# Kernel tuning notes

Hardware: AMD Instinct MI355X
Metric: run time of the kernel (lower is better)

The kernel has to match this reference:

```python
import jax, jax.numpy as jnp
import numpy as np

HEADS = 8

def setup_inputs() -> dict:
    key = jax.random.key(0)
    ks = jax.random.split(key, 5)
    B, C, H, W = 2, 256, 64, 64
    dim = C
    x = jax.random.normal(ks[0], (B, C, H, W), dtype=jnp.float32)
    # Linear weights stored as [in, out] so y = x @ W + b
    w_qkv = jax.random.normal(ks[1], (dim, 3 * dim), dtype=jnp.float32) * (dim ** -0.5)
    b_qkv = jax.random.normal(ks[2], (3 * dim,), dtype=jnp.float32) * 0.02
    w_out = jax.random.normal(ks[3], (dim, dim), dtype=jnp.float32) * (dim ** -0.5)
    b_out = jax.random.normal(ks[4], (dim,), dtype=jnp.float32) * 0.02
    return {"x": x, "w_qkv": w_qkv, "b_qkv": b_qkv, "w_out": w_out, "b_out": b_out}

def reference(x, w_qkv, b_qkv, w_out, b_out):
    B, C, H, W = x.shape
    h = HEADS
    d = C // h
    scale = d ** -0.5
    # [B, C, H, W] -> [B, N, C]
    tokens = x.reshape(B, C, H * W).transpose(0, 2, 1)
    qkv = tokens @ w_qkv + b_qkv  # [B, N, 3C]
    q, k, v = jnp.split(qkv, 3, axis=-1)
    def to_heads(t):
        Bn, N, _ = t.shape
        return t.reshape(Bn, N, h, d).transpose(0, 2, 1, 3)  # [B, h, N, d]
    q, k, v = map(to_heads, (q, k, v))
    dots = jnp.einsum('bhnd,bhmd->bhnm', q, k) * scale  # [B, h, N, N]
    attn = jax.nn.softmax(dots, axis=-1)
    out = jnp.einsum('bhnm,bhmd->bhnd', attn, v)  # [B, h, N, d]
    out = out.transpose(0, 2, 1, 3).reshape(B, H * W, C)  # [B, N, C]
    out = out @ w_out + b_out
    return out.transpose(0, 2, 1).reshape(B, C, H, W)
```

## Files before the change

### kernel.cpp

```cpp
#include <hip/hip_runtime.h>

typedef __attribute__((ext_vector_type(8))) short s16x8;
typedef __attribute__((ext_vector_type(4))) short s16x4;
typedef __attribute__((ext_vector_type(4))) float f32x4;
typedef __attribute__((ext_vector_type(2))) unsigned u32x2;

#define MFMA32(a, b, c) __builtin_amdgcn_mfma_f32_16x16x32_bf16((a), (b), (c), 0, 0, 0)

#if __has_builtin(__builtin_amdgcn_mfma_f32_16x16x16bf16_1k)
#define MFMA16K(a, b, c) __builtin_amdgcn_mfma_f32_16x16x16bf16_1k((a), (b), (c), 0, 0, 0)
#else
#define MFMA16K(a, b, c) (c)
#endif

#if __has_builtin(__builtin_amdgcn_exp2f)
#define EXP2F(x) __builtin_amdgcn_exp2f(x)
#else
#define EXP2F(x) __exp2f(x)
#endif

#if __has_builtin(__builtin_amdgcn_rcpf)
#define RCPF(x) __builtin_amdgcn_rcpf(x)
#else
#define RCPF(x) (1.0f / (x))
#endif

#define SL2E 0.25507313f

__device__ __forceinline__ unsigned pkrne(float a, float b) {
  unsigned ua = __builtin_bit_cast(unsigned, a);
  unsigned ub = __builtin_bit_cast(unsigned, b);
  ua += 0x7FFFu + ((ua >> 16) & 1u);
  ub += 0x7FFFu + ((ub >> 16) & 1u);
  return __builtin_amdgcn_perm(ub, ua, 0x07060302u);
}

__device__ __forceinline__ unsigned pktrunc(float a, float b) {
  return __builtin_amdgcn_perm(__builtin_bit_cast(unsigned, b),
                               __builtin_bit_cast(unsigned, a), 0x07060302u);
}

__device__ __forceinline__ unsigned short bfr(float f) {
  unsigned u = __builtin_bit_cast(unsigned, f);
  u += 0x7FFFu + ((u >> 16) & 1u);
  return (unsigned short)(u >> 16);
}

__device__ __forceinline__ float bflo(unsigned u) {
  return __builtin_bit_cast(float, u << 16);
}
__device__ __forceinline__ float bfhi(unsigned u) {
  return __builtin_bit_cast(float, u & 0xFFFF0000u);
}

__global__ __launch_bounds__(256) void prep_kernel(
    const float* __restrict__ x, const float* __restrict__ wqkv,
    const float* __restrict__ wout, ushort* __restrict__ xbf,
    ushort* __restrict__ wT, ushort* __restrict__ woT) {
  const int t = threadIdx.x;
  const int sub = t & 15, grp = t >> 4;
  const int id = blockIdx.x;
  const float* src;
  ushort* dst;
  int src_ld, k0, n0;
  float sc = 1.f;
  if (id < 512) {
    int mt = id & 63, kt = (id >> 6) & 3, b = id >> 8;
    src = x + (size_t)b * 256 * 4096;
    src_ld = 4096;
    dst = xbf + (size_t)b * 4096 * 256;
    k0 = kt * 64;
    n0 = mt * 64;
  } else if (id < 560) {
    int r = id - 512, nt = r % 12, kt = r / 12;
    src = wqkv;
    src_ld = 768;
    dst = wT;
    k0 = kt * 64;
    n0 = nt * 64;
    if (n0 < 256) sc = SL2E;
  } else {
    int r = id - 560, nt = r & 3, kt = r >> 2;
    src = wout;
    src_ld = 256;
    dst = woT;
    k0 = kt * 64;
    n0 = nt * 64;
  }
  const int k = k0 + grp * 4;
  const int n = n0 + sub * 4;
  unsigned d0[4], d1[4];
#pragma unroll
  for (int i = 0; i < 4; ++i) {
    float4 v = *(const float4*)(src + (size_t)(k + i) * src_ld + n);
    d0[i] = pkrne(v.x * sc, v.y * sc);
    d1[i] = pkrne(v.z * sc, v.w * sc);
  }
  u32x2 r0 = {__builtin_amdgcn_perm(d0[1], d0[0], 0x05040100u),
              __builtin_amdgcn_perm(d0[3], d0[2], 0x05040100u)};
  u32x2 r1 = {__builtin_amdgcn_perm(d0[1], d0[0], 0x07060302u),
              __builtin_amdgcn_perm(d0[3], d0[2], 0x07060302u)};
  u32x2 r2 = {__builtin_amdgcn_perm(d1[1], d1[0], 0x05040100u),
              __builtin_amdgcn_perm(d1[3], d1[2], 0x05040100u)};
  u32x2 r3 = {__builtin_amdgcn_perm(d1[1], d1[0], 0x07060302u),
              __builtin_amdgcn_perm(d1[3], d1[2], 0x07060302u)};
  *(u32x2*)(dst + (size_t)(n + 0) * 256 + k) = r0;
  *(u32x2*)(dst + (size_t)(n + 1) * 256 + k) = r1;
  *(u32x2*)(dst + (size_t)(n + 2) * 256 + k) = r2;
  *(u32x2*)(dst + (size_t)(n + 3) * 256 + k) = r3;
}

__global__ __launch_bounds__(256) void qkv_kernel(
    const ushort* __restrict__ xbf, const ushort* __restrict__ wT,
    const float* __restrict__ bq, ushort* __restrict__ QG,
    ushort* __restrict__ KG, ushort* __restrict__ VtG) {
  __shared__ __align__(16) ushort Wl[64][40];
  __shared__ __align__(16) ushort Xl[128][40];
  const int t0 = blockIdx.x * 128;
  const int n0 = blockIdx.y * 64;
  const int t = threadIdx.x;
  const int wid = t >> 6, lane = t & 63;
  const int wy = wid >> 1, wx = wid & 1;
  const int quad = lane >> 4, l16 = lane & 15;
  f32x4 acc[2][4] = {};
  const int wr = t >> 2, wsg = t & 3;
  for (int k0 = 0; k0 < 256; k0 += 32) {
    __syncthreads();
    *(uint4*)&Wl[wr][wsg * 8] =
        *(const uint4*)(wT + (size_t)(n0 + wr) * 256 + k0 + wsg * 8);
#pragma unroll
    for (int i = 0; i < 2; ++i) {
      int fid = t + 256 * i, row = fid >> 2, seg = fid & 3;
      *(uint4*)&Xl[row][seg * 8] =
          *(const uint4*)(xbf + (size_t)(t0 + row) * 256 + k0 + seg * 8);
    }
    __syncthreads();
    s16x8 wf[2], xf[4];
#pragma unroll
    for (int i = 0; i < 2; ++i)
      wf[i] = *(const s16x8*)&Wl[32 * wy + 16 * i + l16][quad * 8];
#pragma unroll
    for (int j = 0; j < 4; ++j)
      xf[j] = *(const s16x8*)&Xl[64 * wx + 16 * j + l16][quad * 8];
#pragma unroll
    for (int i = 0; i < 2; ++i)
#pragma unroll
      for (int j = 0; j < 4; ++j) acc[i][j] = MFMA32(wf[i], xf[j], acc[i][j]);
  }
  if (n0 < 512) {
    ushort* dst = (n0 < 256) ? QG : KG;
    const float bsc = (n0 < 256) ? SL2E : 1.f;
#pragma unroll
    for (int i = 0; i < 2; ++i) {
      int nb = n0 + 32 * wy + 16 * i + 4 * quad;
      float4 b4 = *(const float4*)(bq + nb);
      float bx0 = b4.x * bsc, bx1 = b4.y * bsc, bx2 = b4.z * bsc,
            bx3 = b4.w * bsc;
      int h = ((nb & 255) >> 5);
      int dd0 = nb & 31;
#pragma unroll
      for (int j = 0; j < 4; ++j) {
        int tok = t0 + 64 * wx + 16 * j + l16;
        int b = tok >> 12, tokn = tok & 4095;
        u32x2 pk = {pkrne(acc[i][j][0] + bx0, acc[i][j][1] + bx1),
                    pkrne(acc[i][j][2] + bx2, acc[i][j][3] + bx3)};
        *(u32x2*)(dst + ((size_t)(b * 8 + h) * 4096 + tokn) * 32 + dd0) = pk;
      }
    }
  } else {
#pragma unroll
    for (int i = 0; i < 2; ++i) {
      int nb = n0 + 32 * wy + 16 * i + 4 * quad;
      float4 b4 = *(const float4*)(bq + nb);
      float bb[4] = {b4.x, b4.y, b4.z, b4.w};
#pragma unroll
      for (int r = 0; r < 4; ++r) {
        int nn = nb + r - 512;
        int h = nn >> 5, ddv = nn & 31;
        ushort* vrow = VtG + (size_t)(h * 32 + ddv) * 4096;
#pragma unroll
        for (int j = 0; j < 4; ++j) {
          int tok = t0 + 64 * wx + 16 * j + l16;
          int b = tok >> 12, tokn = tok & 4095;
          vrow[(size_t)b * 8 * 32 * 4096 + tokn] = bfr(acc[i][j][r] + bb[r]);
        }
      }
    }
  }
}

__global__ __launch_bounds__(256, 4) void attn_split(
    const ushort* __restrict__ QG, const ushort* __restrict__ KG,
    const ushort* __restrict__ VtG, ushort* __restrict__ OF0,
    ushort* __restrict__ OFb, float* __restrict__ LF) {
  __shared__ __align__(16) ushort Kl[2][64][40];
  __shared__ __align__(16) ushort Vl[2][32][72];
  const int id = blockIdx.x;
  const int bh = (id & 7) * 2 + ((id >> 3) & 1);
  const int q0 = ((id >> 4) & 15) * 256;
  const int sp = id >> 8;
  const int kt0 = sp * 16;
  const int t = threadIdx.x;
  const int wid = t >> 6, lane = t & 63;
  const int quad = lane >> 4, l16 = lane & 15;
  const size_t base = (size_t)bh * 4096 * 32;
  const ushort* qp = QG + base;
  const ushort* kp = KG + base;
  const ushort* vp = VtG + base;
  const int qw = q0 + 64 * wid;
  s16x8 qf[4];
#pragma unroll
  for (int f = 0; f < 4; ++f)
    qf[f] = *(const s16x8*)(qp + (size_t)(qw + 16 * f + l16) * 32 + quad * 8);
  const int kr = t >> 2, ks = t & 3;
  const int vr = t >> 3, vsg = t & 7;
  *(uint4*)&Kl[0][kr][ks * 8] =
      *(const uint4*)(kp + (size_t)(kt0 * 64 + kr) * 32 + ks * 8);
  *(uint4*)&Vl[0][vr][vsg * 8] =
      *(const uint4*)(vp + (size_t)vr * 4096 + kt0 * 64 + vsg * 8);
  const ushort* kpre = kp + (size_t)((kt0 + 1) * 64 + kr) * 32 + ks * 8;
  const ushort* vpre = vp + (size_t)vr * 4096 + (kt0 + 1) * 64 + vsg * 8;
  __syncthreads();
  f32x4 oA[4], oB[4], ol[4];
#pragma unroll
  for (int f = 0; f < 4; ++f) {
    oA[f] = f32x4{};
    oB[f] = f32x4{};
    ol[f] = f32x4{};
  }
  const f32x4 zero = {};
  const s16x4 ones = {(short)0x3F80, (short)0x3F80, (short)0x3F80,
                      (short)0x3F80};
  for (int i = 0; i < 16; ++i) {
    const int cur = i & 1;
    const bool more = (i + 1) < 16;
    uint4 kv, vv;
    if (more) {
      kv = *(const uint4*)kpre;
      vv = *(const uint4*)vpre;
      kpre += 2048;
      vpre += 64;
    }
#pragma unroll
    for (int nb = 0; nb < 4; ++nb) {
      s16x8 kf = *(const s16x8*)&Kl[cur][16 * nb + l16][quad * 8];
      s16x4 va = *(const s16x4*)&Vl[cur][l16][16 * nb + quad * 4];
      s16x4 vb = *(const s16x4*)&Vl[cur][16 + l16][16 * nb + quad * 4];
#pragma unroll
      for (int f = 0; f < 4; ++f) {
        f32x4 s = MFMA32(kf, qf[f], zero);
        u32x2 pu = {pktrunc(EXP2F(s[0]), EXP2F(s[1])),
                    pktrunc(EXP2F(s[2]), EXP2F(s[3]))};
        s16x4 pv = __builtin_bit_cast(s16x4, pu);
        oA[f] = MFMA16K(va, pv, oA[f]);
        oB[f] = MFMA16K(vb, pv, oB[f]);
        ol[f] = MFMA16K(ones, pv, ol[f]);
      }
    }
    if (more) {
      *(uint4*)&Kl[cur ^ 1][kr][ks * 8] = kv;
      *(uint4*)&Vl[cur ^ 1][vr][vsg * 8] = vv;
    }
    __syncthreads();
  }
  ushort* OFs = (sp == 0) ? OF0 : OFb + (size_t)(sp - 1) * 2097152;
  float* LFs = LF + (size_t)sp * 65536;
#pragma unroll
  for (int f = 0; f < 4; ++f) {
    const int tok = qw + 16 * f + l16;
    const size_t ob = ((size_t)bh * 4096 + tok) * 32;
    u32x2 wA = {pkrne(oA[f][0], oA[f][1]), pkrne(oA[f][2], oA[f][3])};
    u32x2 wB = {pkrne(oB[f][0], oB[f][1]), pkrne(oB[f][2], oB[f][3])};
    *(u32x2*)(OFs + ob + 4 * quad) = wA;
    *(u32x2*)(OFs + ob + 16 + 4 * quad) = wB;
    if (quad == 0) LFs[(size_t)bh * 4096 + tok] = ol[f][0];
  }
}

__global__ __launch_bounds__(256) void proj_split(
    const ushort* __restrict__ OF0, const ushort* __restrict__ OFb,
    const float* __restrict__ LF, const ushort* __restrict__ woT,
    const float* __restrict__ bo, float* __restrict__ out) {
  __shared__ __align__(16) ushort Wl[64][40];
  __shared__ __align__(16) ushort Xl[128][40];
  const int t0 = blockIdx.x * 128;
  const int c0 = blockIdx.y * 64;
  const int t = threadIdx.x;
  const int wid = t >> 6, lane = t & 63;
  const int wy = wid >> 1, wx = wid & 1;
  const int quad = lane >> 4, l16 = lane & 15;
  f32x4 acc[2][4] = {};
  const int wr = t >> 2, wsg = t & 3;
  const int c8 = (t & 7) * 4;
  for (int k0 = 0; k0 < 256; k0 += 32) {
    __syncthreads();
    *(uint4*)&Wl[wr][wsg * 8] =
        *(const uint4*)(woT + (size_t)(c0 + wr) * 256 + k0 + wsg * 8);
    const int hh = k0 >> 5;
#pragma unroll
    for (int p = 0; p < 4; ++p) {
      int row = 32 * p + (t >> 3);
      int tok = t0 + row, bb = tok >> 12, tokn = tok & 4095;
      size_t ro = (size_t)(bb * 8 + hh) * 4096 + tokn;
      size_t oi = ro * 32 + c8;
      uint2 a0 = *(const uint2*)(OF0 + oi);
      uint2 a1 = *(const uint2*)(OFb + oi);
      uint2 a2 = *(const uint2*)(OFb + 2097152 + oi);
      uint2 a3 = *(const uint2*)(OFb + 4194304 + oi);
      float l = (LF[ro] + LF[65536 + ro]) + (LF[131072 + ro] + LF[196608 + ro]);
      float inv = RCPF(l);
      f32x4 s;
      s[0] = (bflo(a0.x) + bflo(a1.x)) + (bflo(a2.x) + bflo(a3.x));
      s[1] = (bfhi(a0.x) + bfhi(a1.x)) + (bfhi(a2.x) + bfhi(a3.x));
      s[2] = (bflo(a0.y) + bflo(a1.y)) + (bflo(a2.y) + bflo(a3.y));
      s[3] = (bfhi(a0.y) + bfhi(a1.y)) + (bfhi(a2.y) + bfhi(a3.y));
      s *= inv;
      u32x2 pk = {pkrne(s[0], s[1]), pkrne(s[2], s[3])};
      *(u32x2*)&Xl[row][c8] = pk;
    }
    __syncthreads();
    s16x8 wf[2], xf[4];
#pragma unroll
    for (int i = 0; i < 2; ++i)
      wf[i] = *(const s16x8*)&Wl[32 * wy + 16 * i + l16][quad * 8];
#pragma unroll
    for (int j = 0; j < 4; ++j)
      xf[j] = *(const s16x8*)&Xl[64 * wx + 16 * j + l16][quad * 8];
#pragma unroll
    for (int i = 0; i < 2; ++i)
#pragma unroll
      for (int j = 0; j < 4; ++j) acc[i][j] = MFMA32(wf[i], xf[j], acc[i][j]);
  }
#pragma unroll
  for (int i = 0; i < 2; ++i) {
    int cb = c0 + 32 * wy + 16 * i + 4 * quad;
    float4 b4 = *(const float4*)(bo + cb);
    float bb[4] = {b4.x, b4.y, b4.z, b4.w};
#pragma unroll
    for (int j = 0; j < 4; ++j) {
      int tok = t0 + 64 * wx + 16 * j + l16;
      int b = tok >> 12, tokn = tok & 4095;
#pragma unroll
      for (int r = 0; r < 4; ++r)
        out[((size_t)(b * 256 + cb + r)) * 4096 + tokn] = acc[i][j][r] + bb[r];
    }
  }
}

extern "C" void kernel_launch(void* const* d_in, const int* in_sizes, int n_in,
                              void* d_out, int out_size, void* d_ws, size_t ws_size,
                              hipStream_t stream) {
  (void)in_sizes; (void)n_in; (void)out_size; (void)ws_size;
  const float* x = (const float*)d_in[0];
  const float* wq = (const float*)d_in[1];
  const float* bq = (const float*)d_in[2];
  const float* wo = (const float*)d_in[3];
  const float* bo = (const float*)d_in[4];
  float* out = (float*)d_out;
  ushort* ws = (ushort*)d_ws;
  ushort* xbf = ws;
  ushort* OF0 = ws;
  ushort* QG  = ws + 2097152;
  ushort* KG  = ws + 4194304;
  ushort* VtG = ws + 6291456;
  ushort* wT  = ws + 8388608;
  ushort* woT = ws + 8585216;
  ushort* OFb = ws + 8650752;
  float* LF = (float*)(ws + 14942208);
  prep_kernel<<<576, 256, 0, stream>>>(x, wq, wo, xbf, wT, woT);
  qkv_kernel<<<dim3(64, 12), 256, 0, stream>>>(xbf, wT, bq, QG, KG, VtG);
  attn_split<<<1024, 256, 0, stream>>>(QG, KG, VtG, OF0, OFb, LF);
  proj_split<<<dim3(64, 4), 256, 0, stream>>>(OF0, OFb, LF, woT, bo, out);
}
```

Before: 142.9 us.

## Load K/V fragments directly from global memory, dropping LDS staging and barriers

The attention kernel no longer stages K and V tiles through double-buffered shared memory with per-iteration __syncthreads. Each wave now reads its MFMA K and V fragments straight from global memory, relying on L1/L2 caching, with a per-block rotation of the key-tile order to spread accesses across blocks. The goal is to remove the LDS round trip and barrier stalls and to free LDS for occupancy. In exchange, each wave re-fetches the same K/V data its siblings fetch, and the strided V reads (4096-element row stride) may hit the cache poorly and raise global latency.

```diff
diff --git a/kernel.cpp b/kernel.cpp
--- a/kernel.cpp
+++ b/kernel.cpp
@@ -193,13 +193,12 @@
     const ushort* __restrict__ QG, const ushort* __restrict__ KG,
     const ushort* __restrict__ VtG, ushort* __restrict__ OF0,
     ushort* __restrict__ OFb, float* __restrict__ LF) {
-  __shared__ __align__(16) ushort Kl[2][64][40];
-  __shared__ __align__(16) ushort Vl[2][32][72];
   const int id = blockIdx.x;
   const int bh = (id & 7) * 2 + ((id >> 3) & 1);
   const int q0 = ((id >> 4) & 15) * 256;
   const int sp = id >> 8;
   const int kt0 = sp * 16;
+  const int rot = id & 15;
   const int t = threadIdx.x;
   const int wid = t >> 6, lane = t & 63;
   const int quad = lane >> 4, l16 = lane & 15;
@@ -212,15 +211,6 @@
 #pragma unroll
   for (int f = 0; f < 4; ++f)
     qf[f] = *(const s16x8*)(qp + (size_t)(qw + 16 * f + l16) * 32 + quad * 8);
-  const int kr = t >> 2, ks = t & 3;
-  const int vr = t >> 3, vsg = t & 7;
-  *(uint4*)&Kl[0][kr][ks * 8] =
-      *(const uint4*)(kp + (size_t)(kt0 * 64 + kr) * 32 + ks * 8);
-  *(uint4*)&Vl[0][vr][vsg * 8] =
-      *(const uint4*)(vp + (size_t)vr * 4096 + kt0 * 64 + vsg * 8);
-  const ushort* kpre = kp + (size_t)((kt0 + 1) * 64 + kr) * 32 + ks * 8;
-  const ushort* vpre = vp + (size_t)vr * 4096 + (kt0 + 1) * 64 + vsg * 8;
-  __syncthreads();
   f32x4 oA[4], oB[4], ol[4];
 #pragma unroll
   for (int f = 0; f < 4; ++f) {
@@ -231,21 +221,19 @@
   const f32x4 zero = {};
   const s16x4 ones = {(short)0x3F80, (short)0x3F80, (short)0x3F80,
                       (short)0x3F80};
+#pragma unroll 2
   for (int i = 0; i < 16; ++i) {
-    const int cur = i & 1;
-    const bool more = (i + 1) < 16;
-    uint4 kv, vv;
-    if (more) {
-      kv = *(const uint4*)kpre;
-      vv = *(const uint4*)vpre;
-      kpre += 2048;
-      vpre += 64;
-    }
+    const int kt = kt0 + ((i + rot) & 15);
+    const ushort* kbase = kp + (size_t)kt * 64 * 32;
+    const ushort* vbase = vp + kt * 64;
 #pragma unroll
     for (int nb = 0; nb < 4; ++nb) {
-      s16x8 kf = *(const s16x8*)&Kl[cur][16 * nb + l16][quad * 8];
-      s16x4 va = *(const s16x4*)&Vl[cur][l16][16 * nb + quad * 4];
-      s16x4 vb = *(const s16x4*)&Vl[cur][16 + l16][16 * nb + quad * 4];
+      s16x8 kf =
+          *(const s16x8*)(kbase + (size_t)(nb * 16 + l16) * 32 + quad * 8);
+      s16x4 va =
+          *(const s16x4*)(vbase + (size_t)l16 * 4096 + nb * 16 + quad * 4);
+      s16x4 vb = *(const s16x4*)(vbase + (size_t)(16 + l16) * 4096 + nb * 16 +
+                                 quad * 4);
 #pragma unroll
       for (int f = 0; f < 4; ++f) {
         f32x4 s = MFMA32(kf, qf[f], zero);
@@ -257,11 +245,6 @@
         ol[f] = MFMA16K(ones, pv, ol[f]);
       }
     }
-    if (more) {
-      *(uint4*)&Kl[cur ^ 1][kr][ks * 8] = kv;
-      *(uint4*)&Vl[cur ^ 1][vr][vsg * 8] = vv;
-    }
-    __syncthreads();
   }
   ushort* OFs = (sp == 0) ? OF0 : OFb + (size_t)(sp - 1) * 2097152;
   float* LFs = LF + (size_t)sp * 65536;
```

Result: slower. 171.3 us (+19.9%).

## Split attention keys into three chunks instead of four, batch QK MFMAs

Applied to the files above, without the earlier changes.

The attention kernel now splits the 64 key tiles across three partitions of 21–22 tiles instead of four of 16, launching 768 blocks with a launch bound of 3 blocks per SM. The projection kernel combines three partial outputs and denominators instead of four, and the LF workspace is moved to match. Inside the inner loop, all four QK MFMAs are issued before the exp step and before the PV MFMAs, which is meant to expose more instruction-level parallelism. The intent is fewer partial-result reads and writes plus better MFMA pipelining. The cost is a single wave of 768 blocks that may underfill some CUs, and higher register pressure.

```diff
diff --git a/kernel.cpp b/kernel.cpp
--- a/kernel.cpp
+++ b/kernel.cpp
@@ -189,7 +189,7 @@
   }
 }
 
-__global__ __launch_bounds__(256, 4) void attn_split(
+__global__ __launch_bounds__(256, 3) void attn_split(
     const ushort* __restrict__ QG, const ushort* __restrict__ KG,
     const ushort* __restrict__ VtG, ushort* __restrict__ OF0,
     ushort* __restrict__ OFb, float* __restrict__ LF) {
@@ -199,7 +199,8 @@
   const int bh = (id & 7) * 2 + ((id >> 3) & 1);
   const int q0 = ((id >> 4) & 15) * 256;
   const int sp = id >> 8;
-  const int kt0 = sp * 16;
+  const int kt0 = (sp * 64 + 2) / 3;
+  const int niter = ((sp + 1) * 64 + 2) / 3 - kt0;
   const int t = threadIdx.x;
   const int wid = t >> 6, lane = t & 63;
   const int quad = lane >> 4, l16 = lane & 15;
@@ -231,9 +232,9 @@
   const f32x4 zero = {};
   const s16x4 ones = {(short)0x3F80, (short)0x3F80, (short)0x3F80,
                       (short)0x3F80};
-  for (int i = 0; i < 16; ++i) {
+  for (int i = 0; i < niter; ++i) {
     const int cur = i & 1;
-    const bool more = (i + 1) < 16;
+    const bool more = (i + 1) < niter;
     uint4 kv, vv;
     if (more) {
       kv = *(const uint4*)kpre;
@@ -246,15 +247,21 @@
       s16x8 kf = *(const s16x8*)&Kl[cur][16 * nb + l16][quad * 8];
       s16x4 va = *(const s16x4*)&Vl[cur][l16][16 * nb + quad * 4];
       s16x4 vb = *(const s16x4*)&Vl[cur][16 + l16][16 * nb + quad * 4];
+      f32x4 s[4];
+#pragma unroll
+      for (int f = 0; f < 4; ++f) s[f] = MFMA32(kf, qf[f], zero);
+      s16x4 pv[4];
 #pragma unroll
       for (int f = 0; f < 4; ++f) {
-        f32x4 s = MFMA32(kf, qf[f], zero);
-        u32x2 pu = {pktrunc(EXP2F(s[0]), EXP2F(s[1])),
-                    pktrunc(EXP2F(s[2]), EXP2F(s[3]))};
-        s16x4 pv = __builtin_bit_cast(s16x4, pu);
-        oA[f] = MFMA16K(va, pv, oA[f]);
-        oB[f] = MFMA16K(vb, pv, oB[f]);
-        ol[f] = MFMA16K(ones, pv, ol[f]);
+        u32x2 pu = {pktrunc(EXP2F(s[f][0]), EXP2F(s[f][1])),
+                    pktrunc(EXP2F(s[f][2]), EXP2F(s[f][3]))};
+        pv[f] = __builtin_bit_cast(s16x4, pu);
+      }
+#pragma unroll
+      for (int f = 0; f < 4; ++f) {
+        oA[f] = MFMA16K(va, pv[f], oA[f]);
+        oB[f] = MFMA16K(vb, pv[f], oB[f]);
+        ol[f] = MFMA16K(ones, pv[f], ol[f]);
       }
     }
     if (more) {
@@ -306,14 +313,13 @@
       uint2 a0 = *(const uint2*)(OF0 + oi);
       uint2 a1 = *(const uint2*)(OFb + oi);
       uint2 a2 = *(const uint2*)(OFb + 2097152 + oi);
-      uint2 a3 = *(const uint2*)(OFb + 4194304 + oi);
-      float l = (LF[ro] + LF[65536 + ro]) + (LF[131072 + ro] + LF[196608 + ro]);
+      float l = LF[ro] + LF[65536 + ro] + LF[131072 + ro];
       float inv = RCPF(l);
       f32x4 s;
-      s[0] = (bflo(a0.x) + bflo(a1.x)) + (bflo(a2.x) + bflo(a3.x));
-      s[1] = (bfhi(a0.x) + bfhi(a1.x)) + (bfhi(a2.x) + bfhi(a3.x));
-      s[2] = (bflo(a0.y) + bflo(a1.y)) + (bflo(a2.y) + bflo(a3.y));
-      s[3] = (bfhi(a0.y) + bfhi(a1.y)) + (bfhi(a2.y) + bfhi(a3.y));
+      s[0] = bflo(a0.x) + bflo(a1.x) + bflo(a2.x);
+      s[1] = bfhi(a0.x) + bfhi(a1.x) + bfhi(a2.x);
+      s[2] = bflo(a0.y) + bflo(a1.y) + bflo(a2.y);
+      s[3] = bfhi(a0.y) + bfhi(a1.y) + bfhi(a2.y);
       s *= inv;
       u32x2 pk = {pkrne(s[0], s[1]), pkrne(s[2], s[3])};
       *(u32x2*)&Xl[row][c8] = pk;
@@ -366,9 +372,9 @@
   ushort* wT  = ws + 8388608;
   ushort* woT = ws + 8585216;
   ushort* OFb = ws + 8650752;
-  float* LF = (float*)(ws + 14942208);
+  float* LF = (float*)(ws + 12845056);
   prep_kernel<<<576, 256, 0, stream>>>(x, wq, wo, xbf, wT, woT);
   qkv_kernel<<<dim3(64, 12), 256, 0, stream>>>(xbf, wT, bq, QG, KG, VtG);
-  attn_split<<<1024, 256, 0, stream>>>(QG, KG, VtG, OF0, OFb, LF);
+  attn_split<<<768, 256, 0, stream>>>(QG, KG, VtG, OF0, OFb, LF);
   proj_split<<<dim3(64, 4), 256, 0, stream>>>(OF0, OFb, LF, woT, bo, out);
 }
```

After: 142.1 us. About the same (-0.5%).
